# Performance work log

Measured on AMD Instinct MI355X. Metric: run time of the kernel, lower is better.

Reference implementation:

```python
import jax, jax.numpy as jnp
import numpy as np

N, SP, SI, K = 256, 64, 32, 8
CIN, C, HEADS, DH = 32, 128, 8, 16
G = 32
OCC_THRESH = 0.7

def _lrelu(x):
    return jax.nn.leaky_relu(x, 0.01)

def _ln(x):
    mu = x.mean(-1, keepdims=True)
    var = ((x - mu) ** 2).mean(-1, keepdims=True)
    return (x - mu) * jax.lax.rsqrt(var + 1e-5)

def _interp3d(vol, coords):
    # vol [C,D,H,W]; coords [...,3] in (z,y,x) voxel-index units -> [..., C]
    v = jnp.moveaxis(vol, 0, -1)
    Dv, Hv, Wv = v.shape[0], v.shape[1], v.shape[2]
    z = jnp.clip(coords[..., 0], 0.0, Dv - 1.0)
    y = jnp.clip(coords[..., 1], 0.0, Hv - 1.0)
    x = jnp.clip(coords[..., 2], 0.0, Wv - 1.0)
    z0 = jnp.floor(z).astype(jnp.int32); y0 = jnp.floor(y).astype(jnp.int32); x0 = jnp.floor(x).astype(jnp.int32)
    z1 = jnp.minimum(z0 + 1, Dv - 1); y1 = jnp.minimum(y0 + 1, Hv - 1); x1 = jnp.minimum(x0 + 1, Wv - 1)
    wz = (z - z0)[..., None]; wy = (y - y0)[..., None]; wx = (x - x0)[..., None]
    c00 = v[z0, y0, x0] * (1 - wx) + v[z0, y0, x1] * wx
    c01 = v[z0, y1, x0] * (1 - wx) + v[z0, y1, x1] * wx
    c10 = v[z1, y0, x0] * (1 - wx) + v[z1, y0, x1] * wx
    c11 = v[z1, y1, x0] * (1 - wx) + v[z1, y1, x1] * wx
    return (c00 * (1 - wy) + c01 * wy) * (1 - wz) + (c10 * (1 - wy) + c11 * wy) * wz

def _tpoints(T, p):
    return p @ T[:3, :3].T + T[:3, 3]

def _rot(T, v):
    return v @ T[:3, :3].T

def _ray_box(o, d, obj_from_cam, dim):
    oo = _tpoints(obj_from_cam, o); dd = _rot(obj_from_cam, d)
    half = dim / 2
    invd = 1.0 / jnp.where(jnp.abs(dd) < 1e-9, 1e-9, dd)
    t0 = (-half - oo) * invd; t1 = (half - oo) * invd
    tlo = jnp.minimum(t0, t1).max(-1); thi = jnp.maximum(t0, t1).min(-1)
    valid = thi >= jnp.maximum(tlo, 0.0)
    return jnp.where(valid, tlo, jnp.inf)

def _attn_block(x, Wqkv, bqkv, Wo, bo, Wf1, bf1, Wf2, bf2):
    # pre-LN MHA over axis -2, then pre-LN FFN; residuals
    h = _ln(x)
    qkv = h @ Wqkv + bqkv
    q, k, v = jnp.split(qkv, 3, axis=-1)
    hd = lambda a: a.reshape(a.shape[:-1] + (HEADS, DH))
    q, k, v = hd(q), hd(k), hd(v)
    s = jnp.einsum('...qhd,...khd->...hqk', q, k) / jnp.sqrt(jnp.float32(DH))
    a = jax.nn.softmax(s, axis=-1)
    o = jnp.einsum('...hqk,...khd->...qhd', a, v)
    o = o.reshape(o.shape[:-2] + (HEADS * DH,)) @ Wo + bo
    x = x + o
    h = _ln(x)
    return x + (_lrelu(h @ Wf1 + bf1) @ Wf2 + bf2)

def setup_inputs() -> dict:
    key = jax.random.key(0)
    ks = jax.random.split(key, 40)
    d = jnp.concatenate([0.25 * (jax.random.uniform(ks[0], (N, 2)) * 2 - 1), jnp.ones((N, 1))], -1)
    rays_d = d / jnp.linalg.norm(d, axis=-1, keepdims=True)
    rays_o = jnp.zeros((N, 3))
    pose = jnp.eye(4).at[2, 3].set(2.0)
    dimension = jnp.ones((3,))
    w = lambda k_, sh: 0.05 * jax.random.normal(k_, sh)
    return {
        'rays_o': rays_o, 'rays_d': rays_d, 'pose': pose, 'dimension': dimension,
        'voxel_probs': jax.random.uniform(ks[1], (G, G, G)),
        'feature_vol': 0.5 * jax.random.normal(ks[2], (CIN, G, G, G)),
        'feature_vol_highres': 0.5 * jax.random.normal(ks[3], (K, 6, G, G, G)),
        'u_primary': jax.random.uniform(ks[4], (N, SP)),
        'u_cat': jax.random.uniform(ks[5], (N, SI)),
        'u_lam': jax.random.uniform(ks[6], (N, SI)),
        'dW1': w(ks[7], (CIN + 1, C)), 'db1': jnp.zeros((C,)),
        'dW2': w(ks[8], (C, 1)), 'db2': jnp.zeros((1,)),
        'rW0': w(ks[9], (CIN + 10, C)), 'rb0': jnp.zeros((C,)),
        'nf_qkv': w(ks[10], (C, 3 * C)), 'nf_qkvb': jnp.zeros((3 * C,)),
        'nf_o': w(ks[11], (C, C)), 'nf_ob': jnp.zeros((C,)),
        'nf_f1': w(ks[12], (C, 2 * C)), 'nf_f1b': jnp.zeros((2 * C,)),
        'nf_f2': w(ks[13], (2 * C, C)), 'nf_f2b': jnp.zeros((C,)),
        'rt_qkv': w(ks[14], (C, 3 * C)), 'rt_qkvb': jnp.zeros((3 * C,)),
        'rt_o': w(ks[15], (C, C)), 'rt_ob': jnp.zeros((C,)),
        'rt_f1': w(ks[16], (C, 2 * C)), 'rt_f1b': jnp.zeros((2 * C,)),
        'rt_f2': w(ks[17], (2 * C, C)), 'rt_f2b': jnp.zeros((C,)),
        'fW': w(ks[18], (C, 3)), 'fb': jnp.zeros((3,)),
        'n_samples_primary': SP, 'n_samples_importance': SI,
    }

def reference(rays_o, rays_d, pose, dimension, voxel_probs, feature_vol, feature_vol_highres,
              u_primary, u_cat, u_lam,
              dW1, db1, dW2, db2, rW0, rb0,
              nf_qkv, nf_qkvb, nf_o, nf_ob, nf_f1, nf_f1b, nf_f2, nf_f2b,
              rt_qkv, rt_qkvb, rt_o, rt_ob, rt_f1, rt_f1b, rt_f2, rt_f2b,
              fW, fb, n_samples_primary, n_samples_importance):
    SPn, SIn = n_samples_primary, n_samples_importance
    ofc = jnp.linalg.inv(pose)  # obj_from_cam
    t_near = _ray_box(rays_o, rays_d, ofc, dimension)
    t_max = t_near + 10.0 * jnp.abs(dimension).sum()
    p_max = rays_o + t_max[:, None] * rays_d
    t_far = t_max - _ray_box(p_max, -rays_d, ofc, dimension)
    m = jnp.isfinite(t_near) & jnp.isfinite(t_far) & (t_far > t_near)
    tn = jnp.where(m, t_near, 0.0); tf = jnp.where(m, t_far, 1.0)
    # stratified primary samples within [t_near, t_far]
    t_coarse = tn[:, None] + (tf - tn)[:, None] * (jnp.arange(SPn, dtype=jnp.float32) + u_primary) / SPn
    get_pts = lambda t: rays_o[:, None] + t[..., None] * rays_d[:, None]
    p_coarse = get_pts(t_coarse)
    def ncoords(p, shp):
        uvz = 0.5 + _tpoints(ofc, p) / dimension
        return uvz[..., ::-1] * (jnp.array(shp, jnp.float32) - 1.0)
    occ_coarse = _interp3d(voxel_probs[None], ncoords(p_coarse, voxel_probs.shape))[..., 0]
    x_coarse = _interp3d(feature_vol, ncoords(p_coarse, feature_vol.shape[-3:]))
    # importance sampling via inverse CDF over adjacent-bin occupancy
    probs = jnp.clip(occ_coarse[:, :-1] + occ_coarse[:, 1:], 1e-12, None)
    cdf = jnp.cumsum(probs, -1)
    cdf = cdf / cdf[:, -1:]
    inds = jnp.clip((u_cat[:, :, None] >= cdf[:, None, :]).sum(-1), 0, SPn - 2)
    t_fine = u_lam * jnp.take_along_axis(t_coarse, inds, -1) + (1 - u_lam) * jnp.take_along_axis(t_coarse, inds + 1, -1)
    p_fine = get_pts(t_fine)
    occ_fine = _interp3d(voxel_probs[None], ncoords(p_fine, voxel_probs.shape))[..., 0]
    x_fine = _interp3d(feature_vol, ncoords(p_fine, feature_vol.shape[-3:]))
    # merge + sort along sample axis
    t_all = jnp.concatenate([t_coarse, t_fine], -1)
    perm = jnp.argsort(t_all, -1)
    t = jnp.take_along_axis(t_all, perm, -1)
    occ = jnp.take_along_axis(jnp.concatenate([occ_coarse, occ_fine], -1), perm, -1)
    p = jnp.take_along_axis(jnp.concatenate([p_coarse, p_fine], -2), perm[..., None], -2)
    x = jnp.take_along_axis(jnp.concatenate([x_coarse, x_fine], -2), perm[..., None], -2)
    # density MLP
    xx = jnp.concatenate([x, occ[..., None]], -1)
    sigma = jax.nn.sigmoid((_lrelu(xx @ dW1 + db1) @ dW2 + db2)[..., 0])
    occ = jnp.where(occ < OCC_THRESH, 0.0, occ)
    alpha = occ * sigma
    # high-res per-view features
    coords_hr = ncoords(p, feature_vol_highres.shape[-3:])
    x_hr = jax.vmap(_interp3d, in_axes=(0, None))(feature_vol_highres, coords_hr)  # [K,N,S,6]
    x_hr = jnp.moveaxis(x_hr, 0, -2)  # [N,S,K,6]
    R = ofc[:3, :3]
    rdo = rays_d @ R.T
    Kv = x_hr.shape[-2]
    bs = x.shape[:2]
    xx2 = jnp.concatenate([
        jnp.broadcast_to(x[:, :, None, :], bs + (Kv, x.shape[-1])),
        x_hr[..., 0:3],
        x_hr[..., 3:6] @ R.T,
        jnp.broadcast_to(rdo[:, None, None, :], bs + (Kv, 3)),
        jnp.broadcast_to(occ[..., None, None], bs + (Kv, 1)),
    ], -1)  # [N,S,K,CIN+10]
    h = xx2 @ rW0 + rb0
    h = _attn_block(h, nf_qkv, nf_qkvb, nf_o, nf_ob, nf_f1, nf_f1b, nf_f2, nf_f2b)  # over views K
    h = h.mean(-2)  # [N,S,C]
    h = _attn_block(h, rt_qkv, rt_qkvb, rt_o, rt_ob, rt_f1, rt_f1b, rt_f2, rt_f2b)  # over samples S
    radiance = jax.nn.sigmoid(h @ fW + fb)  # [N,S,3]
    mk = m[:, None]
    t = jnp.where(mk, t, 0.0)
    occ = jnp.where(mk, occ, 0.0)
    alpha = jnp.where(mk, alpha, 0.0)
    radiance = jnp.where(m[:, None, None], radiance, 0.0)
    # trailing object axis (n_objects=1), matching movedim(0,-1)
    return t[..., None], alpha[..., None], occ[..., None], radiance[..., None]
```

## Files before the change

kernel.cpp:

```cpp
#include <hip/hip_runtime.h>
#include <hip/hip_bf16.h>
#include <cmath>


using bf16 = __hip_bfloat16;
#define DEV __device__ __forceinline__

typedef __attribute__((ext_vector_type(8))) short short8;
typedef __attribute__((ext_vector_type(4))) float f32x4;

DEV float s2f(short s){ unsigned u=((unsigned)(unsigned short)s)<<16; float f; __builtin_memcpy(&f,&u,4); return f; }
DEV short f2s(float f){ bf16 h=__float2bfloat16(f); short r; __builtin_memcpy(&r,&h,2); return r; }

constexpr int NRAY=256, SP=64, SI=32, S=96, KHR=8, CIN=32, C=128, NH=8, DH=16;
constexpr int NT = NRAY*S;
constexpr int MTOT = NT*KHR;

constexpr size_t OFF_RI=0, OFF_TR=9, OFF_M=16, OFF_TN=272, OFF_TF=528, OFF_RDO=784,
  OFF_TS=1552, OFF_OCCS=26128, OFF_OCCT=50704, OFF_CRD=75280, OFF_XS=149008, F32_CNT=935440;

constexpr size_t WT_W0=0, WT_NQKV=8192, WT_NO=57344, WT_NF1=73728, WT_NF2=106496,
  WT_RQKV=139264, WT_RO=188416, WT_RF1=204800, WT_RF2=237568, WT_TOT=270336;
constexpr size_t H2OFF=WT_TOT;
constexpr size_t CHB=H2OFF+(size_t)NT*128;
constexpr size_t RT_TOT=(size_t)NT*512;

struct Corn { int off[8]; float wz, wy, wx; };

DEV void make_corners(float cz, float cy, float cx, Corn& Cn){
  cz=fminf(fmaxf(cz,0.f),31.f); cy=fminf(fmaxf(cy,0.f),31.f); cx=fminf(fmaxf(cx,0.f),31.f);
  int z0=(int)cz, y0=(int)cy, x0=(int)cx;
  int z1=(z0+1<31)?z0+1:31, y1=(y0+1<31)?y0+1:31, x1=(x0+1<31)?x0+1:31;
  Cn.wz=cz-(float)z0; Cn.wy=cy-(float)y0; Cn.wx=cx-(float)x0;
  int zy00=z0*1024+y0*32, zy01=z0*1024+y1*32, zy10=z1*1024+y0*32, zy11=z1*1024+y1*32;
  Cn.off[0]=zy00+x0; Cn.off[1]=zy00+x1;
  Cn.off[2]=zy01+x0; Cn.off[3]=zy01+x1;
  Cn.off[4]=zy10+x0; Cn.off[5]=zy10+x1;
  Cn.off[6]=zy11+x0; Cn.off[7]=zy11+x1;
}

DEV float interp1(const float* __restrict__ vol, const Corn& Cn){
  float v000=vol[Cn.off[0]], v001=vol[Cn.off[1]];
  float v010=vol[Cn.off[2]], v011=vol[Cn.off[3]];
  float v100=vol[Cn.off[4]], v101=vol[Cn.off[5]];
  float v110=vol[Cn.off[6]], v111=vol[Cn.off[7]];
  float wx=Cn.wx, wy=Cn.wy, wz=Cn.wz;
  float c00=v000*(1.f-wx)+v001*wx, c01=v010*(1.f-wx)+v011*wx;
  float c10=v100*(1.f-wx)+v101*wx, c11=v110*(1.f-wx)+v111*wx;
  return (c00*(1.f-wy)+c01*wy)*(1.f-wz) + (c10*(1.f-wy)+c11*wy)*wz;
}

DEV float ray_box(const float* Ri, const float* tr, const float* o3, const float* d3, const float* half){
  float tlo=-INFINITY, thi=INFINITY;
  for(int j=0;j<3;j++){
    float oo=Ri[j*3+0]*o3[0]+Ri[j*3+1]*o3[1]+Ri[j*3+2]*o3[2]+tr[j];
    float dd=Ri[j*3+0]*d3[0]+Ri[j*3+1]*d3[1]+Ri[j*3+2]*d3[2];
    if (fabsf(dd)<1e-9f) dd=1e-9f;
    float inv=1.f/dd;
    float t0=(-half[j]-oo)*inv, t1=(half[j]-oo)*inv;
    tlo=fmaxf(tlo,fminf(t0,t1)); thi=fminf(thi,fmaxf(t0,t1));
  }
  bool valid = thi >= fmaxf(tlo,0.f);
  return valid ? tlo : INFINITY;
}

__global__ __launch_bounds__(64) void k0_setup(
  const float* __restrict__ rays_o, const float* __restrict__ rays_d,
  const float* __restrict__ pose, const float* __restrict__ dimv,
  float* __restrict__ wsf)
{
  __shared__ float Ri[9], tr[3];
  int tid=threadIdx.x; int ray=blockIdx.x*64+tid;
  if(tid==0){
    float P[16];
    for(int j=0;j<16;j++) P[j]=pose[j];
    float a00=P[0],a01=P[1],a02=P[2],a10=P[4],a11=P[5],a12=P[6],a20=P[8],a21=P[9],a22=P[10];
    float c00=a11*a22-a12*a21, c01=a12*a20-a10*a22, c02=a10*a21-a11*a20;
    float det=a00*c00+a01*c01+a02*c02;
    float id=1.f/det;
    Ri[0]=c00*id; Ri[1]=(a02*a21-a01*a22)*id; Ri[2]=(a01*a12-a02*a11)*id;
    Ri[3]=c01*id; Ri[4]=(a00*a22-a02*a20)*id; Ri[5]=(a02*a10-a00*a12)*id;
    Ri[6]=c02*id; Ri[7]=(a01*a20-a00*a21)*id; Ri[8]=(a00*a11-a01*a10)*id;
    float t0=P[3],t1=P[7],t2=P[11];
    tr[0]=-(Ri[0]*t0+Ri[1]*t1+Ri[2]*t2);
    tr[1]=-(Ri[3]*t0+Ri[4]*t1+Ri[5]*t2);
    tr[2]=-(Ri[6]*t0+Ri[7]*t1+Ri[8]*t2);
    if(blockIdx.x==0){
      for(int j=0;j<9;j++) wsf[OFF_RI+j]=Ri[j];
      for(int j=0;j<3;j++) wsf[OFF_TR+j]=tr[j];
    }
  }
  __syncthreads();
  float o3[3],d3[3],dim[3],half[3];
  for(int j=0;j<3;j++){ o3[j]=rays_o[ray*3+j]; d3[j]=rays_d[ray*3+j];
                        dim[j]=dimv[j]; half[j]=0.5f*dim[j]; }
  float tnear=ray_box(Ri,tr,o3,d3,half);
  float tmax=tnear+10.f*(fabsf(dim[0])+fabsf(dim[1])+fabsf(dim[2]));
  float pm[3]={o3[0]+tmax*d3[0], o3[1]+tmax*d3[1], o3[2]+tmax*d3[2]};
  float nd[3]={-d3[0],-d3[1],-d3[2]};
  float tfar=tmax-ray_box(Ri,tr,pm,nd,half);
  bool mm = isfinite(tnear)&&isfinite(tfar)&&(tfar>tnear);
  wsf[OFF_M+ray]=mm?1.f:0.f;
  wsf[OFF_TN+ray]=mm?tnear:0.f;
  wsf[OFF_TF+ray]=mm?tfar:1.f;
  for(int j=0;j<3;j++)
    wsf[OFF_RDO+(size_t)ray*3+j]=Ri[j*3+0]*d3[0]+Ri[j*3+1]*d3[1]+Ri[j*3+2]*d3[2];
}

__global__ __launch_bounds__(128) void k1_sample(
  const float* __restrict__ rays_o, const float* __restrict__ rays_d, const float* __restrict__ dimv,
  const float* __restrict__ voxel, const float* __restrict__ fvol,
  const float* __restrict__ u_p, const float* __restrict__ u_cat, const float* __restrict__ u_lam,
  float* __restrict__ wsf)
{
  int i=blockIdx.x, tid=threadIdx.x;
  __shared__ float Ri[9], tr[3], dim[3], o3[3], d3[3];
  __shared__ float t_all[S], occ_all[S], crd_sh[S][3];
  __shared__ int   coff[S][8];
  __shared__ float cww[S][3];
  __shared__ float cdf[SP];
  __shared__ float totv;
  __shared__ int   rnk[S];
  if(tid<9) Ri[tid]=wsf[OFF_RI+tid];
  if(tid<3){ tr[tid]=wsf[OFF_TR+tid]; dim[tid]=dimv[tid];
             o3[tid]=rays_o[i*3+tid]; d3[tid]=rays_d[i*3+tid]; }
  __syncthreads();
  float tn=wsf[OFF_TN+i], tf=wsf[OFF_TF+i];

  auto do_sample=[&](int s, float t){
    float px=o3[0]+t*d3[0], py=o3[1]+t*d3[1], pz=o3[2]+t*d3[2];
    float q0=Ri[0]*px+Ri[1]*py+Ri[2]*pz+tr[0];
    float q1=Ri[3]*px+Ri[4]*py+Ri[5]*pz+tr[1];
    float q2=Ri[6]*px+Ri[7]*py+Ri[8]*pz+tr[2];
    float cz=(0.5f+q2/dim[2])*31.f;
    float cy=(0.5f+q1/dim[1])*31.f;
    float cx=(0.5f+q0/dim[0])*31.f;
    crd_sh[s][0]=cz; crd_sh[s][1]=cy; crd_sh[s][2]=cx;
    Corn Cn; make_corners(cz,cy,cx,Cn);
    for(int q=0;q<8;q++) coff[s][q]=Cn.off[q];
    cww[s][0]=Cn.wz; cww[s][1]=Cn.wy; cww[s][2]=Cn.wx;
    occ_all[s]=interp1(voxel,Cn);
    t_all[s]=t;
  };

  if(tid<SP){
    float u=u_p[i*SP+tid];
    float t=tn+(tf-tn)*((float)tid+u)*(1.f/64.f);
    do_sample(tid,t);
  }
  __syncthreads();
  if(tid==0){
    float c=0;
    for(int j=0;j<SP-1;j++){ float pr=occ_all[j]+occ_all[j+1]; pr=fmaxf(pr,1e-12f); c+=pr; cdf[j]=c; }
    totv=c;
  }
  __syncthreads();
  if(tid<SP-1) cdf[tid]=cdf[tid]/totv;
  __syncthreads();
  if(tid<SI){
    float u=u_cat[i*SI+tid];
    int cnt=0;
    for(int j=0;j<SP-1;j++) cnt += (u>=cdf[j])?1:0;
    int ind=(cnt<SP-2)?cnt:(SP-2);
    float lam=u_lam[i*SI+tid];
    float tfine=lam*t_all[ind]+(1.f-lam)*t_all[ind+1];
    do_sample(SP+tid,tfine);
  }
  __syncthreads();
  if(tid<S){
    float ts=t_all[tid]; int r=0;
    for(int j=0;j<S;j++){ float tj=t_all[j]; r += (tj<ts || (tj==ts && j<tid)) ? 1:0; }
    rnk[tid]=r;
    size_t base=(size_t)i*S+r;
    wsf[OFF_TS+base]=ts;
    wsf[OFF_OCCS+base]=occ_all[tid];
    wsf[OFF_CRD+base*3+0]=crd_sh[tid][0];
    wsf[OFF_CRD+base*3+1]=crd_sh[tid][1];
    wsf[OFF_CRD+base*3+2]=crd_sh[tid][2];
  }
  __syncthreads();
  for(int idx=tid; idx<S*CIN; idx+=128){
    int s=idx>>5, c=idx&31;
    float wz=cww[s][0], wy=cww[s][1], wx=cww[s][2];
    const float* vc=fvol+(size_t)c*32768;
    float v000=vc[coff[s][0]], v001=vc[coff[s][1]];
    float v010=vc[coff[s][2]], v011=vc[coff[s][3]];
    float v100=vc[coff[s][4]], v101=vc[coff[s][5]];
    float v110=vc[coff[s][6]], v111=vc[coff[s][7]];
    float c00=v000*(1.f-wx)+v001*wx, c01=v010*(1.f-wx)+v011*wx;
    float c10=v100*(1.f-wx)+v101*wx, c11=v110*(1.f-wx)+v111*wx;
    float val=(c00*(1.f-wy)+c01*wy)*(1.f-wz)+(c10*(1.f-wy)+c11*wy)*wz;
    wsf[OFF_XS+((size_t)i*S+rnk[s])*CIN+c]=val;
  }
}

__global__ __launch_bounds__(128) void k2_sigma(
  const float* __restrict__ dW1, const float* __restrict__ db1,
  const float* __restrict__ dW2, const float* __restrict__ db2,
  float* __restrict__ wsf, float* __restrict__ out)
{
  int t=blockIdx.x, tid=threadIdx.x, i=t/S;
  __shared__ float xx[33];
  __shared__ float part[2];
  if(tid<32) xx[tid]=wsf[OFF_XS+(size_t)t*32+tid];
  if(tid==32) xx[32]=wsf[OFF_OCCS+t];
  __syncthreads();
  float acc=db1[tid];
  for(int k=0;k<33;k++) acc=fmaf(xx[k], dW1[k*C+tid], acc);
  acc = acc>=0.f?acc:0.01f*acc;
  float g = acc*dW2[tid];
  for(int off=32;off;off>>=1) g+=__shfl_down(g,off,64);
  if((tid&63)==0) part[tid>>6]=g;
  __syncthreads();
  if(tid==0){
    float z=part[0]+part[1]+db2[0];
    float sg=1.f/(1.f+expf(-z));
    float occ=xx[32];
    float occt=occ<0.7f?0.f:occ;
    float alpha=occt*sg;
    float m=wsf[OFF_M+i];
    float ts=wsf[OFF_TS+t];
    out[t]      =m!=0.f?ts:0.f;
    out[NT+t]   =m!=0.f?alpha:0.f;
    out[2*NT+t] =m!=0.f?occt:0.f;
    wsf[OFF_OCCT+t]=occt;
  }
}

__global__ __launch_bounds__(256) void k_wprep(
  const float* __restrict__ w0, const float* __restrict__ nqkv, const float* __restrict__ no_,
  const float* __restrict__ nf1, const float* __restrict__ nf2,
  const float* __restrict__ rqkv, const float* __restrict__ ro_,
  const float* __restrict__ rf1, const float* __restrict__ rf2,
  short* __restrict__ WT)
{
  int gid = blockIdx.x*256+threadIdx.x;
  if(gid>=(int)WT_TOT) return;
  const float* src; int K,N,Kp; int base;
  if(gid<8192){src=w0;K=42;N=128;Kp=64;base=0;}
  else if(gid<57344){src=nqkv;K=128;N=384;Kp=128;base=8192;}
  else if(gid<73728){src=no_;K=128;N=128;Kp=128;base=57344;}
  else if(gid<106496){src=nf1;K=128;N=256;Kp=128;base=73728;}
  else if(gid<139264){src=nf2;K=256;N=128;Kp=256;base=106496;}
  else if(gid<188416){src=rqkv;K=128;N=384;Kp=128;base=139264;}
  else if(gid<204800){src=ro_;K=128;N=128;Kp=128;base=188416;}
  else if(gid<237568){src=rf1;K=128;N=256;Kp=128;base=204800;}
  else {src=rf2;K=256;N=128;Kp=256;base=237568;}
  int local=gid-base; int n=local/Kp, k=local%Kp;
  WT[gid] = (k<K)? f2s(src[(size_t)k*N+n]) : (short)0;
}

__global__ __launch_bounds__(64) void k_build(
  const float* __restrict__ fvhr, const float* __restrict__ wsf,
  short* __restrict__ X2, int tok0)
{
  int tloc=blockIdx.x, tid=threadIdx.x;
  int t=tok0+tloc, i=t/S;
  __shared__ float hr[KHR][6];
  __shared__ float xf[32];
  __shared__ float RiS[9];
  __shared__ float geo[4];
  __shared__ float crd[3];
  if(tid<9) RiS[tid]=wsf[OFF_RI+tid];
  if(tid>=16&&tid<19) crd[tid-16]=wsf[OFF_CRD+(size_t)t*3+(tid-16)];
  if(tid>=32) xf[tid-32]=wsf[OFF_XS+(size_t)t*32+(tid-32)];
  if(tid==9) geo[0]=wsf[OFF_OCCT+t];
  if(tid>=12&&tid<15) geo[1+(tid-12)]=wsf[OFF_RDO+(size_t)i*3+(tid-12)];
  __syncthreads();
  if(tid<48){
    int k=tid/6, ch=tid%6;
    Corn Cn; make_corners(crd[0],crd[1],crd[2],Cn);
    hr[k][ch]=interp1(fvhr+(size_t)(k*6+ch)*32768, Cn);
  }
  __syncthreads();
  for(int idx=tid; idx<512; idx+=64){
    int k=idx>>6, j=idx&63; float v;
    if(j<32) v=xf[j];
    else if(j<35) v=hr[k][j-32];
    else if(j<38){int r=j-35; v=hr[k][3]*RiS[r*3+0]+hr[k][4]*RiS[r*3+1]+hr[k][5]*RiS[r*3+2];}
    else if(j<41) v=geo[1+(j-38)];
    else if(j==41) v=geo[0];
    else v=0.f;
    X2[(size_t)(tloc*8+k)*64 + j]=f2s(v);
  }
}

template<int K, bool LNA, bool ACT, bool RESID>
__global__ __launch_bounds__(256) void gemm_ln(
  const short* __restrict__ A, const short* __restrict__ Bt,
  const float* __restrict__ bias, const short* __restrict__ Rres,
  short* __restrict__ Cg, int N)
{
  static_assert(!LNA || K==128, "LNA requires K==128");
  constexpr int KSA = (K<128)?K:128;
  constexpr int NSA = K/KSA;
  constexpr int LDA = KSA+8;
  constexpr int LDB = 64+8;
  __shared__ short Al[128*LDA];
  __shared__ short Bl[128*LDB];
  const int tid=threadIdx.x;
  const int bm=blockIdx.x*128, bn=blockIdx.y*128;
  const int lane=tid&63, wave=tid>>6;
  const int wm=(wave>>1)*64, wn=(wave&1)*64;
  const int quad=lane>>4, m16=lane&15;
  f32x4 acc[4][4];
  for(int a=0;a<4;a++) for(int b=0;b<4;b++) acc[a][b]=(f32x4){0.f,0.f,0.f,0.f};

  for(int sa=0; sa<NSA; ++sa){
    if(sa>0) __syncthreads();
    constexpr int CH8=KSA/8;
    for(int it=0; it<(128*CH8)/256; ++it){
      int li=it*256+tid; int row=li/CH8, kc=li%CH8;
      short8 v = *(const short8*)(A + (size_t)(bm+row)*K + sa*KSA + kc*8);
      if constexpr(LNA){
        float f[8]; float ls=0.f,lq=0.f;
        for(int e=0;e<8;e++){ f[e]=s2f(v[e]); ls+=f[e]; lq+=f[e]*f[e]; }
        for(int off=8;off;off>>=1){ ls+=__shfl_xor(ls,off,16); lq+=__shfl_xor(lq,off,16); }
        float mu=ls*(1.f/128.f);
        float var=lq*(1.f/128.f)-mu*mu;
        float rs=rsqrtf(var+1e-5f);
        for(int e=0;e<8;e++) v[e]=f2s((f[e]-mu)*rs);
      }
      *(short8*)&Al[row*LDA+kc*8]=v;
    }
    __syncthreads();
    for(int sb=0; sb<KSA/64; ++sb){
      if(sb>0) __syncthreads();
      for(int it=0; it<4; ++it){
        int li=it*256+tid; int row=li>>3, kc=li&7;
        *(short8*)&Bl[row*LDB+kc*8] =
          *(const short8*)(Bt + (size_t)(bn+row)*K + sa*KSA + sb*64 + kc*8);
      }
      __syncthreads();
      for(int kk=0; kk<64; kk+=32){
        int ka = sb*64+kk;
        short8 af[4], bfv[4];
        for(int im=0; im<4; im++)
          af[im] = *(const short8*)&Al[(wm+im*16+m16)*LDA + ka + quad*8];
        for(int in=0; in<4; in++)
          bfv[in] = *(const short8*)&Bl[(wn+in*16+m16)*LDB + kk + quad*8];
        for(int im=0;im<4;im++)
          for(int in=0;in<4;in++)
            acc[im][in] = __builtin_amdgcn_mfma_f32_16x16x32_bf16(af[im], bfv[in], acc[im][in], 0,0,0);
      }
    }
  }
  for(int in=0;in<4;in++){
    int col = bn + wn + in*16 + m16;
    float bv = bias[col];
    for(int im=0;im<4;im++){
      for(int r=0;r<4;r++){
        int grow = bm + wm + im*16 + quad*4 + r;
        float v = acc[im][in][r] + bv;
        if constexpr(ACT) v = v>=0.f? v : 0.01f*v;
        if constexpr(RESID) v += s2f(Rres[(size_t)grow*N + col]);
        Cg[(size_t)grow*N + col] = f2s(v);
      }
    }
  }
}

__global__ __launch_bounds__(256) void nf_qkv_attn(
  const short* __restrict__ A, const short* __restrict__ Bt,
  const float* __restrict__ bias, short* __restrict__ att)
{
  __shared__ short Al[32*136];
  __shared__ short U[384*40];
  short* Bl = U;
  short* Qt = U;
  const int tid=threadIdx.x;
  const int bm=blockIdx.x*32;
  for(int it=0; it<2; ++it){
    int li=it*256+tid; int row=li>>4, kc=li&15;
    short8 v = *(const short8*)(A + (size_t)(bm+row)*128 + kc*8);
    float f[8]; float ls=0.f,lq=0.f;
    for(int e=0;e<8;e++){ f[e]=s2f(v[e]); ls+=f[e]; lq+=f[e]*f[e]; }
    for(int off=8;off;off>>=1){ ls+=__shfl_xor(ls,off,16); lq+=__shfl_xor(lq,off,16); }
    float mu=ls*(1.f/128.f);
    float var=lq*(1.f/128.f)-mu*mu;
    float rs=rsqrtf(var+1e-5f);
    for(int e=0;e<8;e++) v[e]=f2s((f[e]-mu)*rs);
    *(short8*)&Al[row*136+kc*8]=v;
  }
  const int lane=tid&63, wave=tid>>6;
  const int quad=lane>>4, m16=lane&15;
  const int wn=wave*96;
  f32x4 acc[2][6];
  for(int a=0;a<2;a++) for(int b=0;b<6;b++) acc[a][b]=(f32x4){0.f,0.f,0.f,0.f};
  for(int kc2=0;kc2<4;++kc2){
    __syncthreads();
    for(int it=0; it<6; ++it){
      int li=it*256+tid; int row=li>>2, c=li&3;
      *(short8*)&Bl[row*40+c*8] = *(const short8*)(Bt + (size_t)row*128 + kc2*32 + c*8);
    }
    __syncthreads();
    int ka=kc2*32;
    short8 af[2], bfv[6];
    af[0]=*(const short8*)&Al[m16*136 + ka + quad*8];
    af[1]=*(const short8*)&Al[(16+m16)*136 + ka + quad*8];
    for(int in=0;in<6;in++) bfv[in]=*(const short8*)&Bl[(wn+in*16+m16)*40 + quad*8];
    for(int im=0;im<2;im++)
      for(int in=0;in<6;in++)
        acc[im][in]=__builtin_amdgcn_mfma_f32_16x16x32_bf16(af[im],bfv[in],acc[im][in],0,0,0);
  }
  __syncthreads();
  for(int in=0;in<6;in++){
    int col=wn+in*16+m16;
    float bv=bias[col];
    for(int im=0;im<2;im++)
      for(int r=0;r<4;r++)
        Qt[(im*16+quad*4+r)*392+col]=f2s(acc[im][in][r]+bv);
  }
  __syncthreads();
  int tok=tid>>6, h=(tid>>3)&7, q=tid&7;
  const short* base=&Qt[(tok*8)*392 + h*16];
  short8 q0v=*(const short8*)&base[q*392];
  short8 q1v=*(const short8*)&base[q*392+8];
  float qv[16];
  for(int e=0;e<8;e++){ qv[e]=s2f(q0v[e]); qv[8+e]=s2f(q1v[e]); }
  float sc[8]; float mx=-INFINITY;
  for(int j=0;j<8;j++){
    short8 k0=*(const short8*)&base[j*392+128];
    short8 k1=*(const short8*)&base[j*392+136];
    float a=0;
    for(int e=0;e<8;e++) a += qv[e]*s2f(k0[e]) + qv[8+e]*s2f(k1[e]);
    a*=0.25f; sc[j]=a; mx=fmaxf(mx,a);
  }
  float se=0;
  for(int j=0;j<8;j++){ sc[j]=expf(sc[j]-mx); se+=sc[j]; }
  float inv=1.f/se;
  float o[16];
  for(int d=0;d<16;d++) o[d]=0.f;
  for(int j=0;j<8;j++){
    short8 v0=*(const short8*)&base[j*392+256];
    short8 v1=*(const short8*)&base[j*392+264];
    float p=sc[j];
    for(int e=0;e<8;e++){ o[e]=fmaf(p,s2f(v0[e]),o[e]); o[8+e]=fmaf(p,s2f(v1[e]),o[8+e]); }
  }
  short8 o0,o1;
  for(int e=0;e<8;e++){ o0[e]=f2s(o[e]*inv); o1[e]=f2s(o[8+e]*inv); }
  size_t ob=(size_t)(bm+tok*8+q)*128 + h*16;
  *(short8*)(att+ob)=o0;
  *(short8*)(att+ob+8)=o1;
}

__global__ __launch_bounds__(256) void nf_f1f2(
  const short* __restrict__ X1, const short* __restrict__ Bt1, const float* __restrict__ b1,
  const short* __restrict__ Bt2, const float* __restrict__ b2,
  short* __restrict__ H2)
{
  __shared__ short Al[32*136];
  __shared__ short Bl[256*40];
  __shared__ short F1[32*264];
  const int tid=threadIdx.x;
  const int bm=blockIdx.x*32;
  for(int it=0; it<2; ++it){
    int li=it*256+tid; int row=li>>4, kc=li&15;
    short8 v = *(const short8*)(X1 + (size_t)(bm+row)*128 + kc*8);
    float f[8]; float ls=0.f,lq=0.f;
    for(int e=0;e<8;e++){ f[e]=s2f(v[e]); ls+=f[e]; lq+=f[e]*f[e]; }
    for(int off=8;off;off>>=1){ ls+=__shfl_xor(ls,off,16); lq+=__shfl_xor(lq,off,16); }
    float mu=ls*(1.f/128.f);
    float var=lq*(1.f/128.f)-mu*mu;
    float rs=rsqrtf(var+1e-5f);
    for(int e=0;e<8;e++) v[e]=f2s((f[e]-mu)*rs);
    *(short8*)&Al[row*136+kc*8]=v;
  }
  const int lane=tid&63, wave=tid>>6;
  const int quad=lane>>4, m16=lane&15;
  {
    const int wn=wave*64;
    f32x4 acc[2][4];
    for(int a=0;a<2;a++) for(int b=0;b<4;b++) acc[a][b]=(f32x4){0.f,0.f,0.f,0.f};
    for(int kc2=0;kc2<4;++kc2){
      __syncthreads();
      for(int it=0; it<4; ++it){
        int li=it*256+tid; int row=li>>2, c=li&3;
        *(short8*)&Bl[row*40+c*8] = *(const short8*)(Bt1 + (size_t)row*128 + kc2*32 + c*8);
      }
      __syncthreads();
      int ka=kc2*32;
      short8 af[2], bfv[4];
      af[0]=*(const short8*)&Al[m16*136 + ka + quad*8];
      af[1]=*(const short8*)&Al[(16+m16)*136 + ka + quad*8];
      for(int in=0;in<4;in++) bfv[in]=*(const short8*)&Bl[(wn+in*16+m16)*40 + quad*8];
      for(int im=0;im<2;im++)
        for(int in=0;in<4;in++)
          acc[im][in]=__builtin_amdgcn_mfma_f32_16x16x32_bf16(af[im],bfv[in],acc[im][in],0,0,0);
    }
    for(int in=0;in<4;in++){
      int col=wn+in*16+m16;
      float bv=b1[col];
      for(int im=0;im<2;im++)
        for(int r=0;r<4;r++){
          float v=acc[im][in][r]+bv;
          v = v>=0.f? v : 0.01f*v;
          F1[(im*16+quad*4+r)*264+col]=f2s(v);
        }
    }
  }
  __syncthreads();
  {
    const int wn=wave*32;
    f32x4 acc[2][2];
    for(int a=0;a<2;a++) for(int b=0;b<2;b++) acc[a][b]=(f32x4){0.f,0.f,0.f,0.f};
    for(int kc2=0;kc2<8;++kc2){
      __syncthreads();
      for(int it=0; it<2; ++it){
        int li=it*256+tid; int row=li>>2, c=li&3;
        *(short8*)&Bl[row*40+c*8] = *(const short8*)(Bt2 + (size_t)row*256 + kc2*32 + c*8);
      }
      __syncthreads();
      int ka=kc2*32;
      short8 af[2], bfv[2];
      af[0]=*(const short8*)&F1[m16*264 + ka + quad*8];
      af[1]=*(const short8*)&F1[(16+m16)*264 + ka + quad*8];
      for(int in=0;in<2;in++) bfv[in]=*(const short8*)&Bl[(wn+in*16+m16)*40 + quad*8];
      for(int im=0;im<2;im++)
        for(int in=0;in<2;in++)
          acc[im][in]=__builtin_amdgcn_mfma_f32_16x16x32_bf16(af[im],bfv[in],acc[im][in],0,0,0);
    }
    for(int in=0;in<2;in++){
      int col=wn+in*16+m16;
      float bv=b2[col];
      for(int im=0;im<2;im++){
        float s4=0.f;
        for(int r=0;r<4;r++){
          int grow=bm+im*16+quad*4+r;
          float v=acc[im][in][r]+bv + s2f(X1[(size_t)grow*128+col]);
          s4+=v;
        }
        float stok = s4 + __shfl_xor(s4,16,64);
        if((quad&1)==0){
          int tok=((bm+im*16)>>3)+(quad>>1);
          H2[(size_t)tok*128+col]=f2s(stok*0.125f);
        }
      }
    }
  }
}

__global__ __launch_bounds__(256) void rt_attn(const short* __restrict__ qkvb, short* __restrict__ attout){
  int b=blockIdx.x; int i=b&255, h0=(b>>8)*4; int tid=threadIdx.x;
  __shared__ float kh[96][64], vh[96][64];
  for(int idx=tid; idx<1536; idx+=256){
    int kv = idx>=768; int l = idx - kv*768;
    int j = l>>3, c = l&7;
    size_t base = ((size_t)(i*96+j))*384 + h0*16 + (kv?256:128) + c*8;
    short8 x = *(const short8*)(qkvb+base);
    float* dst = kv? &vh[j][c*8] : &kh[j][c*8];
    for(int e=0;e<8;e++) dst[e]=s2f(x[e]);
  }
  __syncthreads();
  int jh=tid>>7, t2=tid&127;
  int hh=t2>>5, lq=t2&31, h=h0+hh, r0=lq*3;
  float q[3][16];
  for(int rr=0;rr<3;rr++){
    size_t qb=((size_t)(i*96+r0+rr))*384 + h*16;
    short8 a=*(const short8*)(qkvb+qb), bq=*(const short8*)(qkvb+qb+8);
    for(int e=0;e<8;e++){ q[rr][e]=s2f(a[e]); q[rr][8+e]=s2f(bq[e]); }
  }
  float acc[3][16]; float se[3]={0.f,0.f,0.f};
  for(int rr=0;rr<3;rr++) for(int d=0;d<16;d++) acc[rr][d]=0.f;
  const float* kb=&kh[jh*48][hh*16];
  const float* vb=&vh[jh*48][hh*16];
  for(int j=0;j<48;j++){
    const float* kj = kb + j*64;
    float s0=0.f,s1=0.f,s2=0.f;
    for(int d=0;d<16;d++){ float kv_=kj[d];
      s0=fmaf(q[0][d],kv_,s0); s1=fmaf(q[1][d],kv_,s1); s2=fmaf(q[2][d],kv_,s2); }
    float p0=expf(s0*0.25f), p1=expf(s1*0.25f), p2=expf(s2*0.25f);
    se[0]+=p0; se[1]+=p1; se[2]+=p2;
    const float* vj = vb + j*64;
    for(int d=0;d<16;d++){ float vv=vj[d];
      acc[0][d]=fmaf(p0,vv,acc[0][d]); acc[1][d]=fmaf(p1,vv,acc[1][d]); acc[2][d]=fmaf(p2,vv,acc[2][d]); }
  }
  __syncthreads();
  float* pacc=(float*)kh;
  float* pse =(float*)vh;
  if(jh==1){
    for(int rr=0;rr<3;rr++){
      for(int d=0;d<16;d++) pacc[(t2*3+rr)*16+d]=acc[rr][d];
      pse[t2*3+rr]=se[rr];
    }
  }
  __syncthreads();
  if(jh==0){
    for(int rr=0;rr<3;rr++){
      float sv = se[rr] + pse[t2*3+rr];
      float inv = 1.f/sv;
      short8 o0,o1;
      for(int e=0;e<8;e++){
        float a0=acc[rr][e]   + pacc[(t2*3+rr)*16+e];
        float a1=acc[rr][8+e] + pacc[(t2*3+rr)*16+8+e];
        o0[e]=f2s(a0*inv); o1[e]=f2s(a1*inv);
      }
      size_t ob=((size_t)(i*96+r0+rr))*128 + h*16;
      *(short8*)(attout+ob)=o0;
      *(short8*)(attout+ob+8)=o1;
    }
  }
}

__global__ __launch_bounds__(256) void k_rad(
  const short* __restrict__ h3, const float* __restrict__ fW, const float* __restrict__ fb,
  const float* __restrict__ wsf, float* __restrict__ out)
{
  int t=blockIdx.x*256+threadIdx.x;
  if(t>=NT) return;
  int i=t/S;
  float a0=fb[0], a1=fb[1], a2=fb[2];
  for(int c=0;c<C;c++){
    float hv=s2f(h3[(size_t)t*C+c]);
    a0=fmaf(hv,fW[c*3+0],a0);
    a1=fmaf(hv,fW[c*3+1],a1);
    a2=fmaf(hv,fW[c*3+2],a2);
  }
  float m=wsf[OFF_M+i];
  float r0=1.f/(1.f+expf(-a0)), r1=1.f/(1.f+expf(-a1)), r2=1.f/(1.f+expf(-a2));
  size_t ob=3*(size_t)NT+(size_t)t*3;
  out[ob+0]=m!=0.f?r0:0.f;
  out[ob+1]=m!=0.f?r1:0.f;
  out[ob+2]=m!=0.f?r2:0.f;
}

extern "C" void kernel_launch(void* const* d_in, const int* in_sizes, int n_in,
                              void* d_out, int out_size, void* d_ws, size_t ws_size,
                              hipStream_t stream) {
  (void)in_sizes; (void)n_in; (void)out_size;
  const float* rays_o =(const float*)d_in[0];
  const float* rays_d =(const float*)d_in[1];
  const float* pose   =(const float*)d_in[2];
  const float* dimv   =(const float*)d_in[3];
  const float* voxel  =(const float*)d_in[4];
  const float* fvol   =(const float*)d_in[5];
  const float* fvhr   =(const float*)d_in[6];
  const float* u_p    =(const float*)d_in[7];
  const float* u_cat  =(const float*)d_in[8];
  const float* u_lam  =(const float*)d_in[9];
  const float* dW1    =(const float*)d_in[10];
  const float* db1    =(const float*)d_in[11];
  const float* dW2    =(const float*)d_in[12];
  const float* db2    =(const float*)d_in[13];
  const float* rW0    =(const float*)d_in[14];
  const float* rb0    =(const float*)d_in[15];
  const float* nf_qkv =(const float*)d_in[16];
  const float* nf_qkvb=(const float*)d_in[17];
  const float* nf_o   =(const float*)d_in[18];
  const float* nf_ob  =(const float*)d_in[19];
  const float* nf_f1  =(const float*)d_in[20];
  const float* nf_f1b =(const float*)d_in[21];
  const float* nf_f2  =(const float*)d_in[22];
  const float* nf_f2b =(const float*)d_in[23];
  const float* rt_qkv =(const float*)d_in[24];
  const float* rt_qkvb=(const float*)d_in[25];
  const float* rt_o   =(const float*)d_in[26];
  const float* rt_ob  =(const float*)d_in[27];
  const float* rt_f1  =(const float*)d_in[28];
  const float* rt_f1b =(const float*)d_in[29];
  const float* rt_f2  =(const float*)d_in[30];
  const float* rt_f2b =(const float*)d_in[31];
  const float* fW     =(const float*)d_in[32];
  const float* fb     =(const float*)d_in[33];

  float* wsf=(float*)d_ws;
  short* wsb=(short*)((char*)d_ws + F32_CNT*4);
  float* out=(float*)d_out;

  int nch=8;
  for(int c=1;c<=8;c<<=1){
    size_t mc_=(size_t)MTOT/c;
    size_t region=mc_*640ULL; if(region<RT_TOT) region=RT_TOT;
    size_t need=F32_CNT*4 + 2ULL*(CHB + region);
    if(need <= ws_size){ nch=c; break; }
  }
  const size_t mc = (size_t)MTOT/nch;
  const int Tc = (int)(mc/8);

  short* WT  = wsb;
  short* H2  = wsb + H2OFF;
  short* arena = wsb + CHB;
  short* o_h0 = arena;
  short* o_x1 = arena + (size_t)128*mc;
  short* o_att= arena + (size_t)512*mc;
  short* o_x2 = arena + (size_t)512*mc;
  short* r_qkv= arena;
  short* r_att= arena + (size_t)384*NT;
  short* r_x  = arena;
  short* r_f1 = arena + (size_t)128*NT;
  short* r_h3 = arena + (size_t)384*NT;

  k0_setup<<<NRAY/64,64,0,stream>>>(rays_o,rays_d,pose,dimv,wsf);
  k1_sample<<<NRAY,128,0,stream>>>(rays_o,rays_d,dimv,voxel,fvol,u_p,u_cat,u_lam,wsf);
  k2_sigma<<<NT,128,0,stream>>>(dW1,db1,dW2,db2,wsf,out);
  k_wprep<<<(int)((WT_TOT+255)/256),256,0,stream>>>(rW0,nf_qkv,nf_o,nf_f1,nf_f2,rt_qkv,rt_o,rt_f1,rt_f2,WT);

  const int mt=(int)(mc/128);
  const int mt32=(int)(mc/32);
  for(int ch=0; ch<nch; ++ch){
    int tok0 = ch*Tc;
    k_build<<<Tc,64,0,stream>>>(fvhr, wsf, o_x2, tok0);
    gemm_ln< 64,false,false,false><<<dim3(mt,1),256,0,stream>>>(o_x2, WT+WT_W0,  rb0,     nullptr, o_h0, 128);
    nf_qkv_attn<<<mt32,256,0,stream>>>(o_h0, WT+WT_NQKV, nf_qkvb, o_att);
    gemm_ln<128,false,false,true ><<<dim3(mt,1),256,0,stream>>>(o_att,WT+WT_NO,  nf_ob,   o_h0,    o_x1, 128);
    nf_f1f2<<<mt32,256,0,stream>>>(o_x1, WT+WT_NF1, nf_f1b, WT+WT_NF2, nf_f2b,
                                   H2+(size_t)tok0*128);
  }

  gemm_ln<128,true ,false,false><<<dim3(NT/128,3),256,0,stream>>>(H2,   WT+WT_RQKV,rt_qkvb, nullptr, r_qkv,384);
  rt_attn<<<NRAY*2,256,0,stream>>>(r_qkv, r_att);
  gemm_ln<128,false,false,true ><<<dim3(NT/128,1),256,0,stream>>>(r_att,WT+WT_RO,  rt_ob,   H2,      r_x,  128);
  gemm_ln<128,true ,true ,false><<<dim3(NT/128,2),256,0,stream>>>(r_x,  WT+WT_RF1, rt_f1b,  nullptr, r_f1, 256);
  gemm_ln<256,false,false,true ><<<dim3(NT/128,1),256,0,stream>>>(r_f1, WT+WT_RF2, rt_f2b,  r_x,     r_h3, 128);
  k_rad<<<NT/256,256,0,stream>>>(r_h3, fW, fb, wsf, out);
}
```

Baseline: 501.7 us.

## Fuse neighbor-attention output projection into QKV-attention kernel and pack build blocks

Merges the per-view attention output projection plus residual into the QKV/attention kernel, so the attention result stays in shared memory and the separate GEMM launch with its global round trip goes away. k_build now processes four tokens per 256-thread block instead of one token per 64-thread block. nf_f1f2 aliases its A and F1 shared buffers to cut LDS use and raise occupancy, adding an extra barrier. The fused kernel takes on a second GEMM phase with more barriers and reloads the residual from global memory.

```diff
diff --git a/kernel.cpp b/kernel.cpp
--- a/kernel.cpp
+++ b/kernel.cpp
@@ -250,36 +250,37 @@
   WT[gid] = (k<K)? f2s(src[(size_t)k*N+n]) : (short)0;
 }
 
-__global__ __launch_bounds__(64) void k_build(
+__global__ __launch_bounds__(256) void k_build(
   const float* __restrict__ fvhr, const float* __restrict__ wsf,
   short* __restrict__ X2, int tok0)
 {
-  int tloc=blockIdx.x, tid=threadIdx.x;
+  int tid=threadIdx.x; int sub=tid>>6, stid=tid&63;
+  int tloc=blockIdx.x*4+sub;
   int t=tok0+tloc, i=t/S;
-  __shared__ float hr[KHR][6];
-  __shared__ float xf[32];
+  __shared__ float hr[4][KHR][6];
+  __shared__ float xf[4][32];
   __shared__ float RiS[9];
-  __shared__ float geo[4];
-  __shared__ float crd[3];
+  __shared__ float geo[4][4];
+  __shared__ float crd[4][3];
   if(tid<9) RiS[tid]=wsf[OFF_RI+tid];
-  if(tid>=16&&tid<19) crd[tid-16]=wsf[OFF_CRD+(size_t)t*3+(tid-16)];
-  if(tid>=32) xf[tid-32]=wsf[OFF_XS+(size_t)t*32+(tid-32)];
-  if(tid==9) geo[0]=wsf[OFF_OCCT+t];
-  if(tid>=12&&tid<15) geo[1+(tid-12)]=wsf[OFF_RDO+(size_t)i*3+(tid-12)];
-  __syncthreads();
-  if(tid<48){
-    int k=tid/6, ch=tid%6;
-    Corn Cn; make_corners(crd[0],crd[1],crd[2],Cn);
-    hr[k][ch]=interp1(fvhr+(size_t)(k*6+ch)*32768, Cn);
-  }
-  __syncthreads();
-  for(int idx=tid; idx<512; idx+=64){
+  if(stid>=16&&stid<19) crd[sub][stid-16]=wsf[OFF_CRD+(size_t)t*3+(stid-16)];
+  if(stid>=32) xf[sub][stid-32]=wsf[OFF_XS+(size_t)t*32+(stid-32)];
+  if(stid==9) geo[sub][0]=wsf[OFF_OCCT+t];
+  if(stid>=12&&stid<15) geo[sub][1+(stid-12)]=wsf[OFF_RDO+(size_t)i*3+(stid-12)];
+  __syncthreads();
+  if(stid<48){
+    int k=stid/6, ch=stid%6;
+    Corn Cn; make_corners(crd[sub][0],crd[sub][1],crd[sub][2],Cn);
+    hr[sub][k][ch]=interp1(fvhr+(size_t)(k*6+ch)*32768, Cn);
+  }
+  __syncthreads();
+  for(int idx=stid; idx<512; idx+=64){
     int k=idx>>6, j=idx&63; float v;
-    if(j<32) v=xf[j];
-    else if(j<35) v=hr[k][j-32];
-    else if(j<38){int r=j-35; v=hr[k][3]*RiS[r*3+0]+hr[k][4]*RiS[r*3+1]+hr[k][5]*RiS[r*3+2];}
-    else if(j<41) v=geo[1+(j-38)];
-    else if(j==41) v=geo[0];
+    if(j<32) v=xf[sub][j];
+    else if(j<35) v=hr[sub][k][j-32];
+    else if(j<38){int r=j-35; v=hr[sub][k][3]*RiS[r*3+0]+hr[sub][k][4]*RiS[r*3+1]+hr[sub][k][5]*RiS[r*3+2];}
+    else if(j<41) v=geo[sub][1+(j-38)];
+    else if(j==41) v=geo[sub][0];
     else v=0.f;
     X2[(size_t)(tloc*8+k)*64 + j]=f2s(v);
   }
@@ -360,12 +361,13 @@
   }
 }
 
-__global__ __launch_bounds__(256) void nf_qkv_attn(
-  const short* __restrict__ A, const short* __restrict__ Bt,
-  const float* __restrict__ bias, short* __restrict__ att)
+__global__ __launch_bounds__(256) void nf_qkv_attn_o(
+  const short* __restrict__ A, const short* __restrict__ Btq,
+  const float* __restrict__ bq, const short* __restrict__ Bto,
+  const float* __restrict__ bo, short* __restrict__ X1)
 {
   __shared__ short Al[32*136];
-  __shared__ short U[384*40];
+  __shared__ short U[15360];
   short* Bl = U;
   short* Qt = U;
   const int tid=threadIdx.x;
@@ -391,7 +393,7 @@
     __syncthreads();
     for(int it=0; it<6; ++it){
       int li=it*256+tid; int row=li>>2, c=li&3;
-      *(short8*)&Bl[row*40+c*8] = *(const short8*)(Bt + (size_t)row*128 + kc2*32 + c*8);
+      *(short8*)&Bl[row*40+c*8] = *(const short8*)(Btq + (size_t)row*128 + kc2*32 + c*8);
     }
     __syncthreads();
     int ka=kc2*32;
@@ -406,7 +408,7 @@
   __syncthreads();
   for(int in=0;in<6;in++){
     int col=wn+in*16+m16;
-    float bv=bias[col];
+    float bv=bq[col];
     for(int im=0;im<2;im++)
       for(int r=0;r<4;r++)
         Qt[(im*16+quad*4+r)*392+col]=f2s(acc[im][in][r]+bv);
@@ -439,9 +441,42 @@
   }
   short8 o0,o1;
   for(int e=0;e<8;e++){ o0[e]=f2s(o[e]*inv); o1[e]=f2s(o[8+e]*inv); }
-  size_t ob=(size_t)(bm+tok*8+q)*128 + h*16;
-  *(short8*)(att+ob)=o0;
-  *(short8*)(att+ob+8)=o1;
+  __syncthreads();
+  {
+    int r = tok*8+q;
+    *(short8*)&U[r*136 + h*16]     = o0;
+    *(short8*)&U[r*136 + h*16 + 8] = o1;
+  }
+  short* Wl = U + 4352;
+  const int wn2 = wave*32;
+  f32x4 acc2[2][2];
+  for(int a=0;a<2;a++) for(int b=0;b<2;b++) acc2[a][b]=(f32x4){0.f,0.f,0.f,0.f};
+  for(int kc2=0;kc2<4;++kc2){
+    __syncthreads();
+    for(int it=0; it<2; ++it){
+      int li=it*256+tid; int row=li>>2, c=li&3;
+      *(short8*)&Wl[row*40+c*8] = *(const short8*)(Bto + (size_t)row*128 + kc2*32 + c*8);
+    }
+    __syncthreads();
+    int ka=kc2*32;
+    short8 af[2], bfv[2];
+    af[0]=*(const short8*)&U[m16*136 + ka + quad*8];
+    af[1]=*(const short8*)&U[(16+m16)*136 + ka + quad*8];
+    for(int in=0;in<2;in++) bfv[in]=*(const short8*)&Wl[(wn2+in*16+m16)*40 + quad*8];
+    for(int im=0;im<2;im++)
+      for(int in=0;in<2;in++)
+        acc2[im][in]=__builtin_amdgcn_mfma_f32_16x16x32_bf16(af[im],bfv[in],acc2[im][in],0,0,0);
+  }
+  for(int in=0;in<2;in++){
+    int col=wn2+in*16+m16;
+    float bv=bo[col];
+    for(int im=0;im<2;im++)
+      for(int r=0;r<4;r++){
+        int grow=bm+im*16+quad*4+r;
+        float v=acc2[im][in][r]+bv + s2f(A[(size_t)grow*128+col]);
+        X1[(size_t)grow*128+col]=f2s(v);
+      }
+  }
 }
 
 __global__ __launch_bounds__(256) void nf_f1f2(
@@ -449,9 +484,10 @@
   const short* __restrict__ Bt2, const float* __restrict__ b2,
   short* __restrict__ H2)
 {
-  __shared__ short Al[32*136];
-  __shared__ short Bl[256*40];
-  __shared__ short F1[32*264];
+  __shared__ short LB[8448 + 10240];
+  short* Al = LB;
+  short* F1 = LB;
+  short* Bl = LB + 8448;
   const int tid=threadIdx.x;
   const int bm=blockIdx.x*32;
   for(int it=0; it<2; ++it){
@@ -488,6 +524,7 @@
         for(int in=0;in<4;in++)
           acc[im][in]=__builtin_amdgcn_mfma_f32_16x16x32_bf16(af[im],bfv[in],acc[im][in],0,0,0);
     }
+    __syncthreads();
     for(int in=0;in<4;in++){
       int col=wn+in*16+m16;
       float bv=b1[col];
@@ -682,7 +719,6 @@
   short* arena = wsb + CHB;
   short* o_h0 = arena;
   short* o_x1 = arena + (size_t)128*mc;
-  short* o_att= arena + (size_t)512*mc;
   short* o_x2 = arena + (size_t)512*mc;
   short* r_qkv= arena;
   short* r_att= arena + (size_t)384*NT;
@@ -699,10 +735,9 @@
   const int mt32=(int)(mc/32);
   for(int ch=0; ch<nch; ++ch){
     int tok0 = ch*Tc;
-    k_build<<<Tc,64,0,stream>>>(fvhr, wsf, o_x2, tok0);
+    k_build<<<Tc/4,256,0,stream>>>(fvhr, wsf, o_x2, tok0);
     gemm_ln< 64,false,false,false><<<dim3(mt,1),256,0,stream>>>(o_x2, WT+WT_W0,  rb0,     nullptr, o_h0, 128);
-    nf_qkv_attn<<<mt32,256,0,stream>>>(o_h0, WT+WT_NQKV, nf_qkvb, o_att);
-    gemm_ln<128,false,false,true ><<<dim3(mt,1),256,0,stream>>>(o_att,WT+WT_NO,  nf_ob,   o_h0,    o_x1, 128);
+    nf_qkv_attn_o<<<mt32,256,0,stream>>>(o_h0, WT+WT_NQKV, nf_qkvb, WT+WT_NO, nf_ob, o_x1);
     nf_f1f2<<<mt32,256,0,stream>>>(o_x1, WT+WT_NF1, nf_f1b, WT+WT_NF2, nf_f2b,
                                    H2+(size_t)tok0*128);
   }
```

Measured after the change: 466.4 us (median of 3 runs). 7.0% less time.
